# Kernel optimization log

Hardware: AMD Instinct MI355X
Metric: run time of the kernel (lower is better)

## Reference

```python
import jax, jax.numpy as jnp
import numpy as np

N_NODES = 50000
N_EDGES = 800000
D_IN = 128
D_OUT = 128


def setup_inputs() -> dict:
    key = jax.random.key(0)
    k1, k2, k3, k4, k5 = jax.random.split(key, 5)
    feature = jax.random.normal(k1, (N_NODES, D_IN), dtype=jnp.float32)
    src = jax.random.randint(k2, (N_EDGES,), 0, N_NODES, dtype=jnp.int32)
    dst = jax.random.randint(k3, (N_EDGES,), 0, N_NODES, dtype=jnp.int32)
    # nn.Linear default init scale ~ 1/sqrt(in_feats)
    W = jax.random.normal(k4, (D_OUT, D_IN), dtype=jnp.float32) / np.sqrt(D_IN)
    b = jax.random.normal(k5, (D_OUT,), dtype=jnp.float32) / np.sqrt(D_IN)
    return {"feature": feature, "src": src, "dst": dst, "W": W, "b": b}


def reference(feature, src, dst, W, b):
    # update_all(copy_src, sum): gather source node features per edge,
    # scatter-add into destination nodes -> [N, D_IN]
    msgs = feature[src]  # [E, D_IN]
    agg = jax.ops.segment_sum(msgs, dst, num_segments=N_NODES)
    # apply_nodes: linear + activation
    z = jax.nn.relu(agg @ W.T + b)
    # residual: in_feats == out_feats -> identity down path
    return z + feature
```

## Files before the change

kernel.cpp:

```cpp
#include <hip/hip_runtime.h>

#define N_NODES 50000
#define N_EDGES 800000
#define D 128
#define CAP 64

typedef unsigned short ushort_t;
typedef unsigned int uint_t;
typedef __attribute__((ext_vector_type(8))) short bf16x8;
typedef __attribute__((ext_vector_type(4))) float f32x4;

#define WS_COUNTS 0
#define WS_ESRC   50048
#define WS_FB16   (WS_ESRC + N_NODES*CAP)
#define WS_WB16   (WS_FB16 + N_NODES*D/2)
#define WS_FULL_BYTES  ((size_t)(WS_WB16 + D * D / 2) * 4)
#define WS_CSR_BYTES   ((size_t)(WS_ESRC + N_NODES * CAP) * 4)

__device__ inline uint_t pack2bf16(float lo, float hi) {
  uint_t ulo = __builtin_bit_cast(uint_t, lo);
  uint_t uhi = __builtin_bit_cast(uint_t, hi);
  ulo = (ulo + 0x7fffu + ((ulo >> 16) & 1u)) >> 16;
  uhi = (uhi + 0x7fffu + ((uhi >> 16) & 1u)) & 0xffff0000u;
  return ulo | uhi;
}

__global__ __launch_bounds__(256) void prep_kernel(
    const float* __restrict__ f, const float* __restrict__ W,
    int* __restrict__ counts, ushort_t* __restrict__ fb,
    ushort_t* __restrict__ wb) {
  const int i = blockIdx.x * 256 + threadIdx.x;
  if (i < N_NODES * D / 8) {
    const float4 v0 = ((const float4*)f)[2 * i];
    const float4 v1 = ((const float4*)f)[2 * i + 1];
    uint_t r[4];
    r[0] = pack2bf16(v0.x, v0.y);
    r[1] = pack2bf16(v0.z, v0.w);
    r[2] = pack2bf16(v1.x, v1.y);
    r[3] = pack2bf16(v1.z, v1.w);
    *(uint4*)(fb + (size_t)i * 8) = *(const uint4*)r;
  }
  if (i < D * D / 8) {
    const float4 v0 = ((const float4*)W)[2 * i];
    const float4 v1 = ((const float4*)W)[2 * i + 1];
    uint_t r[4];
    r[0] = pack2bf16(v0.x, v0.y);
    r[1] = pack2bf16(v0.z, v0.w);
    r[2] = pack2bf16(v1.x, v1.y);
    r[3] = pack2bf16(v1.z, v1.w);
    *(uint4*)(wb + (size_t)i * 8) = *(const uint4*)r;
  }
  if (i < 50048) counts[i] = 0;
}

__global__ __launch_bounds__(256) void build_kernel(const int* __restrict__ src,
                                                    const int* __restrict__ dst,
                                                    int* __restrict__ counts,
                                                    int* __restrict__ esrc) {
  const int e = blockIdx.x * 256 + threadIdx.x;
  if (e < N_EDGES) {
    const int d = dst[e];
    const int pos = atomicAdd(&counts[d], 1);
    if (pos < CAP) esrc[(size_t)d * CAP + pos] = src[e];
  }
}

#define RPB 32
__global__ __launch_bounds__(256) void gather_transform_kernel(
    const float* __restrict__ feature,
    const ushort_t* __restrict__ fb16,
    const ushort_t* __restrict__ wb16,
    const int* __restrict__ counts,
    const int* __restrict__ esrc,
    const float* __restrict__ b,
    float* __restrict__ out) {
  __shared__ float sA[RPB][D + 4];

  const int tid  = threadIdx.x;
  const int row0 = blockIdx.x * RPB;
  const int l = tid & 15;
  const int g = tid >> 4;

#pragma unroll
  for (int p = 0; p < 2; ++p) {
    const int r   = p * 16 + g;
    const int row = row0 + r;
    float a[8];
#pragma unroll
    for (int k = 0; k < 8; ++k) a[k] = 0.f;
    if (row < N_NODES) {
      int cnt = counts[row];
      if (cnt > CAP) cnt = CAP;
      const size_t base = (size_t)row * CAP;
      for (int j0 = 0; j0 < cnt; j0 += 16) {
        int eid = 0;
        if (j0 + l < cnt) eid = esrc[base + j0 + l];
        const int lim = (cnt - j0 < 16) ? (cnt - j0) : 16;
        if (lim == 16) {
#pragma unroll
          for (int k = 0; k < 16; ++k) {
            const int s = __shfl(eid, k, 16);
            const uint4 w4 = *(const uint4*)(fb16 + (size_t)s * D + l * 8);
            const uint_t ws[4] = {w4.x, w4.y, w4.z, w4.w};
#pragma unroll
            for (int q = 0; q < 4; ++q) {
              a[2 * q]     += __builtin_bit_cast(float, ws[q] << 16);
              a[2 * q + 1] += __builtin_bit_cast(float, ws[q] & 0xffff0000u);
            }
          }
        } else {
          for (int k = 0; k < lim; ++k) {
            const int s = __shfl(eid, k, 16);
            const uint4 w4 = *(const uint4*)(fb16 + (size_t)s * D + l * 8);
            const uint_t ws[4] = {w4.x, w4.y, w4.z, w4.w};
#pragma unroll
            for (int q = 0; q < 4; ++q) {
              a[2 * q]     += __builtin_bit_cast(float, ws[q] << 16);
              a[2 * q + 1] += __builtin_bit_cast(float, ws[q] & 0xffff0000u);
            }
          }
        }
      }
    }
    float4* sp = (float4*)&sA[r][l * 8];
    sp[0] = make_float4(a[0], a[1], a[2], a[3]);
    sp[1] = make_float4(a[4], a[5], a[6], a[7]);
  }
  __syncthreads();

  const int wave = tid >> 6;
  const int lane = tid & 63;
  const int lr = lane & 15;
  const int lk = lane >> 4;

  f32x4 acc00 = {0.f, 0.f, 0.f, 0.f}, acc01 = acc00;
  f32x4 acc10 = acc00, acc11 = acc00;

#pragma unroll
  for (int ks = 0; ks < 4; ++ks) {
    bf16x8 afr[2];
#pragma unroll
    for (int mt = 0; mt < 2; ++mt) {
      const float* ap = &sA[mt * 16 + lr][ks * 32 + lk * 8];
      const float4 a0 = *(const float4*)ap;
      const float4 a1 = *(const float4*)(ap + 4);
      uint_t u[4];
      u[0] = pack2bf16(a0.x, a0.y);
      u[1] = pack2bf16(a0.z, a0.w);
      u[2] = pack2bf16(a1.x, a1.y);
      u[3] = pack2bf16(a1.z, a1.w);
      afr[mt] = __builtin_bit_cast(bf16x8, *(const uint4*)u);
    }
    bf16x8 bfr[2];
#pragma unroll
    for (int ntl = 0; ntl < 2; ++ntl) {
      const int col = (2 * wave + ntl) * 16 + lr;
      bfr[ntl] = *(const bf16x8*)(wb16 + (size_t)col * D + ks * 32 + lk * 8);
    }
    acc00 = __builtin_amdgcn_mfma_f32_16x16x32_bf16(afr[0], bfr[0], acc00, 0, 0, 0);
    acc01 = __builtin_amdgcn_mfma_f32_16x16x32_bf16(afr[0], bfr[1], acc01, 0, 0, 0);
    acc10 = __builtin_amdgcn_mfma_f32_16x16x32_bf16(afr[1], bfr[0], acc10, 0, 0, 0);
    acc11 = __builtin_amdgcn_mfma_f32_16x16x32_bf16(afr[1], bfr[1], acc11, 0, 0, 0);
  }

#pragma unroll
  for (int mt = 0; mt < 2; ++mt) {
#pragma unroll
    for (int ntl = 0; ntl < 2; ++ntl) {
      const f32x4 av = (mt == 0) ? (ntl == 0 ? acc00 : acc01)
                                 : (ntl == 0 ? acc10 : acc11);
      const int col = (2 * wave + ntl) * 16 + lr;
      const float bias = b[col];
#pragma unroll
      for (int j = 0; j < 4; ++j) {
        const int row = row0 + mt * 16 + lk * 4 + j;
        if (row < N_NODES) {
          const size_t o = (size_t)row * D + col;
          float z = av[j] + bias;
          z = z > 0.f ? z : 0.f;
          out[o] = z + feature[o];
        }
      }
    }
  }
}

__global__ __launch_bounds__(256) void gather_transform_f32_kernel(
    const float* __restrict__ feature,
    const int* __restrict__ counts,
    const int* __restrict__ esrc,
    const float* __restrict__ W,
    const float* __restrict__ b,
    float* __restrict__ out) {
  __shared__ float sA[RPB][D];
  const int tid  = threadIdx.x;
  const int row0 = blockIdx.x * RPB;
  const int l = tid & 15;
  const int g = tid >> 4;
#pragma unroll
  for (int p = 0; p < 2; ++p) {
    const int r   = p * 16 + g;
    const int row = row0 + r;
    float4 a0 = make_float4(0.f, 0.f, 0.f, 0.f);
    float4 a1 = make_float4(0.f, 0.f, 0.f, 0.f);
    if (row < N_NODES) {
      int cnt = counts[row];
      if (cnt > CAP) cnt = CAP;
      const size_t base = (size_t)row * CAP;
      for (int j0 = 0; j0 < cnt; j0 += 16) {
        int eid = 0;
        if (j0 + l < cnt) eid = esrc[base + j0 + l];
        const int lim = (cnt - j0 < 16) ? (cnt - j0) : 16;
        for (int k = 0; k < lim; ++k) {
          const int s = __shfl(eid, k, 16);
          const float* fp = feature + (size_t)s * D + l * 8;
          const float4 v0 = *(const float4*)fp;
          const float4 v1 = *(const float4*)(fp + 4);
          a0.x += v0.x; a0.y += v0.y; a0.z += v0.z; a0.w += v0.w;
          a1.x += v1.x; a1.y += v1.y; a1.z += v1.z; a1.w += v1.w;
        }
      }
    }
    float4* sp = (float4*)&sA[r][l * 8];
    sp[0] = a0; sp[1] = a1;
  }
  __syncthreads();
  const int c  = tid & 127;
  const int rh = tid >> 7;
  float acc[16];
#pragma unroll
  for (int r = 0; r < 16; ++r) acc[r] = 0.f;
  for (int k = 0; k < D; ++k) {
    const float wv = W[c * D + k];
#pragma unroll
    for (int r = 0; r < 16; ++r) acc[r] += sA[rh * 16 + r][k] * wv;
  }
  const float bias = b[c];
#pragma unroll
  for (int r = 0; r < 16; ++r) {
    const int row = row0 + rh * 16 + r;
    if (row < N_NODES) {
      const size_t o = (size_t)row * D + c;
      float z = acc[r] + bias;
      z = z > 0.f ? z : 0.f;
      out[o] = z + feature[o];
    }
  }
}

__global__ __launch_bounds__(256) void scatter_kernel(
    const float* __restrict__ feature,
    const int* __restrict__ src,
    const int* __restrict__ dst,
    float* __restrict__ agg) {
  const long long total = (long long)N_EDGES * (D / 4);
  long long idx = (long long)blockIdx.x * blockDim.x + threadIdx.x;
  const long long stride = (long long)gridDim.x * blockDim.x;
  for (; idx < total; idx += stride) {
    const int e  = (int)(idx >> 5);
    const int c4 = ((int)idx & 31) * 4;
    const float4 v = *(const float4*)(feature + (long long)src[e] * D + c4);
    float* p = agg + (long long)dst[e] * D + c4;
    atomicAdd(p + 0, v.x);
    atomicAdd(p + 1, v.y);
    atomicAdd(p + 2, v.z);
    atomicAdd(p + 3, v.w);
  }
}

__global__ __launch_bounds__(256) void transform_kernel(
    float* __restrict__ agg_out,
    const float* __restrict__ feature,
    const float* __restrict__ W,
    const float* __restrict__ b) {
  __shared__ float sA[RPB][D];
  const int row0 = blockIdx.x * RPB;
  for (int i = threadIdx.x; i < RPB * (D / 4); i += 256) {
    const int r  = i >> 5;
    const int c4 = (i & 31) * 4;
    const int row = row0 + r;
    float4 v = make_float4(0.f, 0.f, 0.f, 0.f);
    if (row < N_NODES) v = *(const float4*)(agg_out + (long long)row * D + c4);
    *(float4*)&sA[r][c4] = v;
  }
  __syncthreads();
  const int c  = threadIdx.x & 127;
  const int rh = threadIdx.x >> 7;
  float acc[16];
#pragma unroll
  for (int r = 0; r < 16; ++r) acc[r] = 0.f;
  for (int k = 0; k < D; ++k) {
    const float wv = W[c * D + k];
#pragma unroll
    for (int r = 0; r < 16; ++r) acc[r] += sA[rh * 16 + r][k] * wv;
  }
  const float bias = b[c];
#pragma unroll
  for (int r = 0; r < 16; ++r) {
    const int row = row0 + rh * 16 + r;
    if (row < N_NODES) {
      const long long o = (long long)row * D + c;
      float z = acc[r] + bias;
      z = z > 0.f ? z : 0.f;
      agg_out[o] = z + feature[o];
    }
  }
}

extern "C" void kernel_launch(void* const* d_in, const int* in_sizes, int n_in,
                              void* d_out, int out_size, void* d_ws, size_t ws_size,
                              hipStream_t stream) {
  const float* feature = (const float*)d_in[0];
  const int*   src     = (const int*)d_in[1];
  const int*   dst     = (const int*)d_in[2];
  const float* W       = (const float*)d_in[3];
  const float* b       = (const float*)d_in[4];
  float* out = (float*)d_out;

  const int eblocks = (N_EDGES + 255) / 256;
  const int nblocks = (N_NODES + RPB - 1) / RPB;

  if (ws_size >= WS_FULL_BYTES) {
    int*      wsi    = (int*)d_ws;
    int*      counts = wsi + WS_COUNTS;
    int*      esrc   = wsi + WS_ESRC;
    ushort_t* fb16   = (ushort_t*)(wsi + WS_FB16);
    ushort_t* wb16   = (ushort_t*)(wsi + WS_WB16);

    prep_kernel<<<eblocks, 256, 0, stream>>>(feature, W, counts, fb16, wb16);
    build_kernel<<<eblocks, 256, 0, stream>>>(src, dst, counts, esrc);
    gather_transform_kernel<<<nblocks, 256, 0, stream>>>(feature, fb16, wb16,
                                                         counts, esrc, b, out);
  } else if (ws_size >= WS_CSR_BYTES) {
    int* wsi    = (int*)d_ws;
    int* counts = wsi + WS_COUNTS;
    int* esrc   = wsi + WS_ESRC;

    hipMemsetAsync(counts, 0, (size_t)N_NODES * 4, stream);
    build_kernel<<<eblocks, 256, 0, stream>>>(src, dst, counts, esrc);
    gather_transform_f32_kernel<<<nblocks, 256, 0, stream>>>(feature, counts,
                                                             esrc, W, b, out);
  } else {
    hipMemsetAsync(out, 0, (size_t)N_NODES * D * sizeof(float), stream);
    scatter_kernel<<<2048, 256, 0, stream>>>(feature, src, dst, out);
    transform_kernel<<<nblocks, 256, 0, stream>>>(out, feature, W, b);
  }
}
```

Before: 189.0 us.

## Split fused gather+MFMA into column-sliced gather kernel and separate transform kernel

The fused gather-plus-matmul kernel is split in two. A new gather kernel processes 64-row tiles, each handled by four 32-column slices. Block indices are interleaved so that blocks reading the same column slice run close together, which aims to improve L2 hit rates on the bf16 feature gathers. The aggregate is written in fp32 to the output buffer, and a second MFMA kernel reads it back, applies the linear layer, bias, relu and residual, and overwrites it in place. This adds an extra global write and read of the aggregate plus another launch, in exchange for better cache locality on the random gathers.

```diff
diff --git a/kernel.cpp b/kernel.cpp
--- a/kernel.cpp
+++ b/kernel.cpp
@@ -65,66 +65,83 @@
   }
 }
 
-#define RPB 32
-__global__ __launch_bounds__(256) void gather_transform_kernel(
-    const float* __restrict__ feature,
+#define GROWS 64
+__global__ __launch_bounds__(256) void gather_slice_kernel(
     const ushort_t* __restrict__ fb16,
-    const ushort_t* __restrict__ wb16,
     const int* __restrict__ counts,
     const int* __restrict__ esrc,
-    const float* __restrict__ b,
-    float* __restrict__ out) {
-  __shared__ float sA[RPB][D + 4];
-
-  const int tid  = threadIdx.x;
-  const int row0 = blockIdx.x * RPB;
-  const int l = tid & 15;
-  const int g = tid >> 4;
-
-#pragma unroll
-  for (int p = 0; p < 2; ++p) {
-    const int r   = p * 16 + g;
-    const int row = row0 + r;
-    float a[8];
-#pragma unroll
-    for (int k = 0; k < 8; ++k) a[k] = 0.f;
-    if (row < N_NODES) {
-      int cnt = counts[row];
-      if (cnt > CAP) cnt = CAP;
-      const size_t base = (size_t)row * CAP;
-      for (int j0 = 0; j0 < cnt; j0 += 16) {
-        int eid = 0;
-        if (j0 + l < cnt) eid = esrc[base + j0 + l];
-        const int lim = (cnt - j0 < 16) ? (cnt - j0) : 16;
-        if (lim == 16) {
-#pragma unroll
-          for (int k = 0; k < 16; ++k) {
-            const int s = __shfl(eid, k, 16);
-            const uint4 w4 = *(const uint4*)(fb16 + (size_t)s * D + l * 8);
-            const uint_t ws[4] = {w4.x, w4.y, w4.z, w4.w};
-#pragma unroll
-            for (int q = 0; q < 4; ++q) {
-              a[2 * q]     += __builtin_bit_cast(float, ws[q] << 16);
-              a[2 * q + 1] += __builtin_bit_cast(float, ws[q] & 0xffff0000u);
-            }
+    float* __restrict__ agg) {
+  const int x     = blockIdx.x & 7;
+  const int j     = blockIdx.x >> 3;
+  const int tile  = j * 2 + (x & 1);
+  const int slice = x >> 1;
+  const int row0  = tile * GROWS;
+  const int l = threadIdx.x & 3;
+  const int g = threadIdx.x >> 2;
+  const int row = row0 + g;
+  const int col0 = slice * 32 + l * 8;
+
+  float a[8];
+#pragma unroll
+  for (int k = 0; k < 8; ++k) a[k] = 0.f;
+
+  if (row < N_NODES) {
+    int cnt = counts[row];
+    if (cnt > CAP) cnt = CAP;
+    const size_t base = (size_t)row * CAP;
+    for (int j0 = 0; j0 < cnt; j0 += 4) {
+      int eid = 0;
+      if (j0 + l < cnt) eid = esrc[base + j0 + l];
+      const int lim = (cnt - j0 < 4) ? (cnt - j0) : 4;
+      if (lim == 4) {
+#pragma unroll
+        for (int k = 0; k < 4; ++k) {
+          const int s = __shfl(eid, k, 4);
+          const uint4 w4 = *(const uint4*)(fb16 + (size_t)s * D + col0);
+          const uint_t ws[4] = {w4.x, w4.y, w4.z, w4.w};
+#pragma unroll
+          for (int q = 0; q < 4; ++q) {
+            a[2 * q]     += __builtin_bit_cast(float, ws[q] << 16);
+            a[2 * q + 1] += __builtin_bit_cast(float, ws[q] & 0xffff0000u);
           }
-        } else {
-          for (int k = 0; k < lim; ++k) {
-            const int s = __shfl(eid, k, 16);
-            const uint4 w4 = *(const uint4*)(fb16 + (size_t)s * D + l * 8);
-            const uint_t ws[4] = {w4.x, w4.y, w4.z, w4.w};
-#pragma unroll
-            for (int q = 0; q < 4; ++q) {
-              a[2 * q]     += __builtin_bit_cast(float, ws[q] << 16);
-              a[2 * q + 1] += __builtin_bit_cast(float, ws[q] & 0xffff0000u);
-            }
+        }
+      } else {
+        for (int k = 0; k < lim; ++k) {
+          const int s = __shfl(eid, k, 4);
+          const uint4 w4 = *(const uint4*)(fb16 + (size_t)s * D + col0);
+          const uint_t ws[4] = {w4.x, w4.y, w4.z, w4.w};
+#pragma unroll
+          for (int q = 0; q < 4; ++q) {
+            a[2 * q]     += __builtin_bit_cast(float, ws[q] << 16);
+            a[2 * q + 1] += __builtin_bit_cast(float, ws[q] & 0xffff0000u);
           }
         }
       }
     }
-    float4* sp = (float4*)&sA[r][l * 8];
-    sp[0] = make_float4(a[0], a[1], a[2], a[3]);
-    sp[1] = make_float4(a[4], a[5], a[6], a[7]);
+    float* p = agg + (size_t)row * D + col0;
+    *(float4*)p       = make_float4(a[0], a[1], a[2], a[3]);
+    *(float4*)(p + 4) = make_float4(a[4], a[5], a[6], a[7]);
+  }
+}
+
+#define RPB 32
+__global__ __launch_bounds__(256) void transform_mfma_kernel(
+    float* __restrict__ agg_out,
+    const float* __restrict__ feature,
+    const ushort_t* __restrict__ wb16,
+    const float* __restrict__ b) {
+  __shared__ float sA[RPB][D + 4];
+
+  const int tid  = threadIdx.x;
+  const int row0 = blockIdx.x * RPB;
+
+  for (int i = tid; i < RPB * (D / 4); i += 256) {
+    const int r  = i >> 5;
+    const int c4 = (i & 31) * 4;
+    const int row = row0 + r;
+    float4 v = make_float4(0.f, 0.f, 0.f, 0.f);
+    if (row < N_NODES) v = *(const float4*)(agg_out + (size_t)row * D + c4);
+    *(float4*)&sA[r][c4] = v;
   }
   __syncthreads();
 
@@ -172,13 +189,13 @@
       const int col = (2 * wave + ntl) * 16 + lr;
       const float bias = b[col];
 #pragma unroll
-      for (int j = 0; j < 4; ++j) {
-        const int row = row0 + mt * 16 + lk * 4 + j;
+      for (int jj = 0; jj < 4; ++jj) {
+        const int row = row0 + mt * 16 + lk * 4 + jj;
         if (row < N_NODES) {
           const size_t o = (size_t)row * D + col;
-          float z = av[j] + bias;
+          float z = av[jj] + bias;
           z = z > 0.f ? z : 0.f;
-          out[o] = z + feature[o];
+          agg_out[o] = z + feature[o];
         }
       }
     }
@@ -329,8 +346,11 @@
 
     prep_kernel<<<eblocks, 256, 0, stream>>>(feature, W, counts, fb16, wb16);
     build_kernel<<<eblocks, 256, 0, stream>>>(src, dst, counts, esrc);
-    gather_transform_kernel<<<nblocks, 256, 0, stream>>>(feature, fb16, wb16,
-                                                         counts, esrc, b, out);
+
+    const int gtiles = (N_NODES + GROWS - 1) / GROWS;
+    const int gje    = (gtiles + 1) / 2;
+    gather_slice_kernel<<<gje * 8, 256, 0, stream>>>(fb16, counts, esrc, out);
+    transform_mfma_kernel<<<nblocks, 256, 0, stream>>>(out, feature, wb16, b);
   } else if (ws_size >= WS_CSR_BYTES) {
     int* wsi    = (int*)d_ws;
     int* counts = wsi + WS_COUNTS;
```

After: 201.9 us. 6.8% more time.
